# Performance work log

Measured on AMD Instinct MI355X. Metric: run time of the kernel, lower is better.

## Reference

```python
import jax, jax.numpy as jnp
import numpy as np

B, N, DIM = 8, 1024, 1024
H, DH = 16, 64           # heads, dim_head; inner_dim = H*DH = 1024
SCALE = DH ** -0.5


def setup_inputs() -> dict:
    key = jax.random.key(0)
    k_x, k_qkv, k_out, k_b = jax.random.split(key, 4)
    inner = H * DH
    x = jax.random.normal(k_x, (B, N, DIM), dtype=jnp.float32)
    # nn.Linear(dim, inner*3, bias=False): y = x @ W_qkv
    W_qkv = jax.random.normal(k_qkv, (DIM, 3 * inner), dtype=jnp.float32) * (DIM ** -0.5)
    # nn.Linear(inner, dim) with bias (project_out is True since heads!=1)
    W_out = jax.random.normal(k_out, (inner, DIM), dtype=jnp.float32) * (inner ** -0.5)
    b_out = jax.random.normal(k_b, (DIM,), dtype=jnp.float32) * 0.01
    return {"x": x, "W_qkv": W_qkv, "W_out": W_out, "b_out": b_out}


def reference(x, W_qkv, W_out, b_out):
    # 'trans' branch of Attention.forward (dropout p=0 -> identity)
    qkv = x @ W_qkv                                   # [b, n, 3*inner]
    q, k, v = jnp.split(qkv, 3, axis=-1)              # each [b, n, inner]
    def to_heads(t):
        b, n, _ = t.shape
        return t.reshape(b, n, H, DH).transpose(0, 2, 1, 3)  # [b, h, n, d]
    q, k, v = to_heads(q), to_heads(k), to_heads(v)
    dots = jnp.einsum('bhid,bhjd->bhij', q, k) * SCALE  # [b, h, n, n]
    attn = jax.nn.softmax(dots, axis=-1)
    out = jnp.einsum('bhij,bhjd->bhid', attn, v)        # [b, h, n, d]
    # original sets attn = out (b h n d) before merging heads
    attn_ret = out
    out_m = out.transpose(0, 2, 1, 3).reshape(B, N, H * DH)  # [b, n, inner]
    proj = out_m @ W_out + b_out                        # [b, n, dim]
    return (proj, attn_ret)
```

## Files before the change

### kernel.cpp

```cpp
#include <hip/hip_runtime.h>
#include <hip/hip_bf16.h>
#include <math.h>

typedef __bf16 bf16_t;
typedef __bf16 bf16x8 __attribute__((ext_vector_type(8)));
typedef __bf16 bf16x4 __attribute__((ext_vector_type(4)));
typedef float f32x4 __attribute__((ext_vector_type(4)));

#define MFMA16(a, b, c) __builtin_amdgcn_mfma_f32_16x16x32_bf16((a), (b), (c), 0, 0, 0)

#define AS3(p) ((__attribute__((address_space(3))) void*)(p))
#define AS1(p) ((const __attribute__((address_space(1))) void*)(p))

#define B_ 8
#define N_ 1024
#define DIM_ 1024
#define H_ 16
#define DH_ 64

#define QSCALE 0.18033688011112042f
#define SM_SHIFT 12.0f

__global__ __launch_bounds__(256) void k_convert(const float* __restrict__ in,
                                                 bf16_t* __restrict__ out) {
    size_t idx = ((size_t)blockIdx.x * 256 + threadIdx.x) * 8;
    f32x4 a = *(const f32x4*)(in + idx);
    f32x4 b = *(const f32x4*)(in + idx + 4);
    bf16x8 o;
    o[0] = (bf16_t)a[0]; o[1] = (bf16_t)a[1]; o[2] = (bf16_t)a[2]; o[3] = (bf16_t)a[3];
    o[4] = (bf16_t)b[0]; o[5] = (bf16_t)b[1]; o[6] = (bf16_t)b[2]; o[7] = (bf16_t)b[3];
    *(bf16x8*)(out + idx) = o;
}

__global__ __launch_bounds__(256) void k_prep_w(const float* __restrict__ Wqkv,
                                                bf16_t* __restrict__ wqkvt,
                                                const float* __restrict__ Wout,
                                                bf16_t* __restrict__ woutt) {
    __shared__ float tile[32][33];
    int bx = blockIdx.x;
    const float* in;
    bf16_t* out;
    int C, cb;
    if (bx < 96) { in = Wqkv; out = wqkvt; C = 3072; cb = bx; }
    else         { in = Wout; out = woutt; C = 1024; cb = bx - 96; }
    const int R = 1024;
    int c0 = cb * 32, r0 = blockIdx.y * 32;
    int tx = threadIdx.x, ty = threadIdx.y;
#pragma unroll
    for (int i = 0; i < 4; ++i)
        tile[ty + 8 * i][tx] = in[(size_t)(r0 + ty + 8 * i) * C + (c0 + tx)];
    __syncthreads();
#pragma unroll
    for (int i = 0; i < 4; ++i)
        out[(size_t)(c0 + ty + 8 * i) * R + (r0 + tx)] = (bf16_t)tile[tx][ty + 8 * i];
}

__global__ __launch_bounds__(512, 2) void k_gemm_qkv(const bf16_t* __restrict__ A,
                                                     const bf16_t* __restrict__ Bt,
                                                     bf16_t* __restrict__ qb,
                                                     bf16_t* __restrict__ kbuf,
                                                     bf16_t* __restrict__ vtb) {
    __shared__ __align__(16) bf16_t As[2][256 * 64];
    __shared__ __align__(16) bf16_t Bs[2][256 * 64];
    int tid = threadIdx.x;
    int lane = tid & 63, wave = tid >> 6;
    int quad = lane >> 4, l16 = lane & 15;
    int wr = wave >> 2, wc = wave & 3;

    int bid = blockIdx.x;
    int swz = (bid & 7) * 48 + (bid >> 3);
    int mt = swz / 12, nt = swz % 12;
    int m0 = mt * 256, c0 = nt * 256;

    const f32x4 vzero = {0.f, 0.f, 0.f, 0.f};
    f32x4 acc[8][4];
#pragma unroll
    for (int i = 0; i < 8; ++i)
#pragma unroll
        for (int j = 0; j < 4; ++j) acc[i][j] = vzero;

    int s0 = ((quad) ^ (l16 & 7)) * 8;
    int s1 = ((4 + quad) ^ (l16 & 7)) * 8;

    auto stage = [&](int t) {
        int k0 = t * 64;
        bf16_t* Ad = &As[t & 1][0];
        bf16_t* Bd = &Bs[t & 1][0];
#pragma unroll
        for (int i = 0; i < 4; ++i) {
            int cid = tid + 512 * i;
            int row = cid >> 3;
            int g = (cid & 7) ^ (row & 7);
            __builtin_amdgcn_global_load_lds(
                AS1(A + (size_t)(m0 + row) * 1024 + k0 + g * 8), AS3(Ad + cid * 8), 16, 0, 0);
        }
#pragma unroll
        for (int i = 0; i < 4; ++i) {
            int cid = tid + 512 * i;
            int row = cid >> 3;
            int g = (cid & 7) ^ (row & 7);
            __builtin_amdgcn_global_load_lds(
                AS1(Bt + (size_t)(c0 + row) * 1024 + k0 + g * 8), AS3(Bd + cid * 8), 16, 0, 0);
        }
    };

    stage(0);
    stage(1);

#pragma unroll 2
    for (int t = 0; t < 16; ++t) {
        int cur = t & 1;
        if (t < 15)
            asm volatile("s_waitcnt vmcnt(8)" ::: "memory");
        else
            asm volatile("s_waitcnt vmcnt(0)" ::: "memory");
        __builtin_amdgcn_s_barrier();
        asm volatile("" ::: "memory");

        const bf16_t* Arow = &As[cur][0] + (size_t)(wr * 128 + l16) * 64;
        const bf16_t* Brow = &Bs[cur][0] + (size_t)(wc * 64 + l16) * 64;

        bf16x8 af[4][2], bq0[2][2], bq1[2][2];

#pragma unroll
        for (int i = 0; i < 4; ++i) {
            af[i][0] = *(const bf16x8*)(Arow + (16 * i) * 64 + s0);
            af[i][1] = *(const bf16x8*)(Arow + (16 * i) * 64 + s1);
        }
#pragma unroll
        for (int j = 0; j < 2; ++j) {
            bq0[j][0] = *(const bf16x8*)(Brow + (16 * j) * 64 + s0);
            bq0[j][1] = *(const bf16x8*)(Brow + (16 * j) * 64 + s1);
        }
        __builtin_amdgcn_s_setprio(1);
#pragma unroll
        for (int i = 0; i < 4; ++i)
#pragma unroll
            for (int j = 0; j < 2; ++j) {
                acc[i][j] = MFMA16(af[i][0], bq0[j][0], acc[i][j]);
                acc[i][j] = MFMA16(af[i][1], bq0[j][1], acc[i][j]);
            }
        __builtin_amdgcn_s_setprio(0);

#pragma unroll
        for (int j = 0; j < 2; ++j) {
            bq1[j][0] = *(const bf16x8*)(Brow + (32 + 16 * j) * 64 + s0);
            bq1[j][1] = *(const bf16x8*)(Brow + (32 + 16 * j) * 64 + s1);
        }
        __builtin_amdgcn_s_setprio(1);
#pragma unroll
        for (int i = 0; i < 4; ++i)
#pragma unroll
            for (int j = 0; j < 2; ++j) {
                acc[i][2 + j] = MFMA16(af[i][0], bq1[j][0], acc[i][2 + j]);
                acc[i][2 + j] = MFMA16(af[i][1], bq1[j][1], acc[i][2 + j]);
            }
        __builtin_amdgcn_s_setprio(0);

#pragma unroll
        for (int i = 0; i < 4; ++i) {
            af[i][0] = *(const bf16x8*)(Arow + (64 + 16 * i) * 64 + s0);
            af[i][1] = *(const bf16x8*)(Arow + (64 + 16 * i) * 64 + s1);
        }
        __builtin_amdgcn_s_setprio(1);
#pragma unroll
        for (int i = 0; i < 4; ++i)
#pragma unroll
            for (int j = 0; j < 2; ++j) {
                acc[4 + i][2 + j] = MFMA16(af[i][0], bq1[j][0], acc[4 + i][2 + j]);
                acc[4 + i][2 + j] = MFMA16(af[i][1], bq1[j][1], acc[4 + i][2 + j]);
            }
        __builtin_amdgcn_s_setprio(0);

        __builtin_amdgcn_s_setprio(1);
#pragma unroll
        for (int i = 0; i < 4; ++i)
#pragma unroll
            for (int j = 0; j < 2; ++j) {
                acc[4 + i][j] = MFMA16(af[i][0], bq0[j][0], acc[4 + i][j]);
                acc[4 + i][j] = MFMA16(af[i][1], bq0[j][1], acc[4 + i][j]);
            }
        __builtin_amdgcn_s_setprio(0);

        asm volatile("" ::: "memory");
        __builtin_amdgcn_s_barrier();
        if (t + 2 < 16) stage(t + 2);
    }

    int tsel = nt >> 2;
#pragma unroll
    for (int i = 0; i < 8; ++i) {
#pragma unroll
        for (int r = 0; r < 4; ++r) {
            int m = m0 + wr * 128 + 16 * i + quad * 4 + r;
            int b = m >> 10, n = m & 1023;
#pragma unroll
            for (int j = 0; j < 4; ++j) {
                int cc = c0 + wc * 64 + 16 * j + l16;
                int ic = cc & 1023;
                int h = ic >> 6, d = ic & 63;
                float val = acc[i][j][r];
                if (tsel == 0)
                    qb[(((size_t)b * H_ + h) * N_ + n) * DH_ + d] = (bf16_t)(val * QSCALE);
                else if (tsel == 1)
                    kbuf[(((size_t)b * H_ + h) * N_ + n) * DH_ + d] = (bf16_t)val;
                else
                    vtb[(((size_t)b * H_ + h) * DH_ + d) * N_ + n] = (bf16_t)val;
            }
        }
    }
}

__global__ __launch_bounds__(256, 2) void k_attn(const bf16_t* __restrict__ q,
                                                 const bf16_t* __restrict__ k,
                                                 const bf16_t* __restrict__ vt,
                                                 float* __restrict__ oattn,
                                                 bf16_t* __restrict__ outm) {
    __shared__ __align__(16) bf16_t Ks[64 * 64];
    __shared__ __align__(16) bf16_t Vs[64 * 64];
    __shared__ __align__(16) bf16_t Ps[4 * 4 * 16 * 72];
    int tid = threadIdx.x;
    int lane = tid & 63, wave = tid >> 6;
    int quad = lane >> 4, l16 = lane & 15;
    int qt = blockIdx.x & 3;
    int bh = blockIdx.x >> 2;
    int b = bh >> 4, h = bh & 15;

    const bf16_t* qp = q + ((size_t)bh * N_ + qt * 256 + wave * 64) * DH_;
    bf16x8 qa[4][2];
#pragma unroll
    for (int g = 0; g < 4; ++g)
#pragma unroll
        for (int c = 0; c < 2; ++c)
            qa[g][c] = *(const bf16x8*)(qp + (size_t)(g * 16 + l16) * DH_ + c * 32 + quad * 8);

    const bf16_t* kp = k + (size_t)bh * N_ * DH_;
    const bf16_t* vp = vt + (size_t)bh * DH_ * N_;
    bf16_t* Pw = Ps + wave * (4 * 16 * 72);

    const f32x4 vzero = {0.f, 0.f, 0.f, 0.f};
    f32x4 o[4][4];
#pragma unroll
    for (int g = 0; g < 4; ++g)
#pragma unroll
        for (int t = 0; t < 4; ++t) o[g][t] = vzero;
    float lsum[4] = {0.f, 0.f, 0.f, 0.f};

    for (int kb = 0; kb < 16; ++kb) {
#pragma unroll
        for (int i = 0; i < 2; ++i) {
            int cid = tid + 256 * i;
            int row = cid >> 3;
            int g = (cid & 7) ^ (row & 7);
            __builtin_amdgcn_global_load_lds(
                AS1(kp + (size_t)(kb * 64 + row) * DH_ + g * 8), AS3(Ks + cid * 8), 16, 0, 0);
            __builtin_amdgcn_global_load_lds(
                AS1(vp + (size_t)row * N_ + kb * 64 + g * 8), AS3(Vs + cid * 8), 16, 0, 0);
        }
        __syncthreads();

        f32x4 st[4][4];
#pragma unroll
        for (int jt = 0; jt < 4; ++jt) {
#pragma unroll
            for (int g = 0; g < 4; ++g) st[g][jt] = vzero;
#pragma unroll
            for (int c = 0; c < 2; ++c) {
                int s = (4 * c + quad) ^ (l16 & 7);
                bf16x8 kf = *(const bf16x8*)(Ks + (16 * jt + l16) * 64 + s * 8);
#pragma unroll
                for (int g = 0; g < 4; ++g)
                    st[g][jt] = MFMA16(kf, qa[g][c], st[g][jt]);
            }
        }

#pragma unroll
        for (int g = 0; g < 4; ++g) {
            float ps = 0.f;
#pragma unroll
            for (int jt = 0; jt < 4; ++jt) {
                bf16x4 pk;
#pragma unroll
                for (int r = 0; r < 4; ++r) {
                    float p = __builtin_amdgcn_exp2f(st[g][jt][r] - SM_SHIFT);
                    ps += p;
                    pk[r] = (bf16_t)p;
                }
                *(bf16x4*)(Pw + g * (16 * 72) + l16 * 72 + jt * 16 + quad * 4) = pk;
            }
            lsum[g] += ps;
        }

        bf16x8 pf[4][2];
#pragma unroll
        for (int g = 0; g < 4; ++g)
#pragma unroll
            for (int c = 0; c < 2; ++c)
                pf[g][c] = *(const bf16x8*)(Pw + g * (16 * 72) + l16 * 72 + c * 32 + quad * 8);
#pragma unroll
        for (int t = 0; t < 4; ++t)
#pragma unroll
            for (int c = 0; c < 2; ++c) {
                int s = (4 * c + quad) ^ (l16 & 7);
                bf16x8 vf = *(const bf16x8*)(Vs + (16 * t + l16) * 64 + s * 8);
#pragma unroll
                for (int g = 0; g < 4; ++g)
                    o[g][t] = MFMA16(vf, pf[g][c], o[g][t]);
            }
        __syncthreads();
    }

#pragma unroll
    for (int g = 0; g < 4; ++g) {
        lsum[g] += __shfl_xor(lsum[g], 16);
        lsum[g] += __shfl_xor(lsum[g], 32);
    }

    float* Ot = (float*)Ps + wave * 16 * 68;
#pragma unroll
    for (int g = 0; g < 4; ++g) {
        float inv = 1.f / lsum[g];
#pragma unroll
        for (int t = 0; t < 4; ++t) {
            f32x4 v4;
#pragma unroll
            for (int r = 0; r < 4; ++r) v4[r] = o[g][t][r] * inv;
            *(f32x4*)(Ot + l16 * 68 + t * 16 + quad * 4) = v4;
        }
        int row = lane >> 2, cl = lane & 3;
        int n = qt * 256 + wave * 64 + g * 16 + row;
        const float* orow = Ot + row * 68 + cl * 16;
        float* gout = oattn + ((size_t)bh * N_ + n) * DH_ + cl * 16;
        bf16_t* gm = outm + ((size_t)b * N_ + n) * DIM_ + h * DH_ + cl * 16;
#pragma unroll
        for (int s = 0; s < 4; ++s) {
            f32x4 v = *(const f32x4*)(orow + s * 4);
            *(f32x4*)(gout + s * 4) = v;
            bf16x4 vb;
#pragma unroll
            for (int r = 0; r < 4; ++r) vb[r] = (bf16_t)v[r];
            *(bf16x4*)(gm + s * 4) = vb;
        }
    }
}

__global__ __launch_bounds__(256) void k_gemm_proj(const bf16_t* __restrict__ A,
                                                   const bf16_t* __restrict__ Bt,
                                                   const float* __restrict__ bias,
                                                   float* __restrict__ out) {
    __shared__ __align__(16) bf16_t As[128 * 64];
    __shared__ __align__(16) bf16_t Bs[128 * 64];
    int tid = threadIdx.x;
    int lane = tid & 63, wave = tid >> 6;
    int quad = lane >> 4, l16 = lane & 15;
    int m0 = blockIdx.y * 128, c0 = blockIdx.x * 128;
    int wm = (wave & 1) * 64, wn = (wave >> 1) * 64;

    const f32x4 vzero = {0.f, 0.f, 0.f, 0.f};
    f32x4 acc[4][4];
#pragma unroll
    for (int i = 0; i < 4; ++i)
#pragma unroll
        for (int j = 0; j < 4; ++j) acc[i][j] = vzero;

    for (int k0 = 0; k0 < 1024; k0 += 64) {
#pragma unroll
        for (int i = 0; i < 4; ++i) {
            int cid = tid + 256 * i;
            int row = cid >> 3;
            int g = (cid & 7) ^ (row & 7);
            __builtin_amdgcn_global_load_lds(
                AS1(A + (size_t)(m0 + row) * 1024 + k0 + g * 8), AS3(As + cid * 8), 16, 0, 0);
            __builtin_amdgcn_global_load_lds(
                AS1(Bt + (size_t)(c0 + row) * 1024 + k0 + g * 8), AS3(Bs + cid * 8), 16, 0, 0);
        }
        __syncthreads();
#pragma unroll
        for (int c = 0; c < 2; ++c) {
            int s = (4 * c + quad) ^ (l16 & 7);
            bf16x8 bfr[4];
#pragma unroll
            for (int j = 0; j < 4; ++j)
                bfr[j] = *(const bf16x8*)(Bs + (wn + 16 * j + l16) * 64 + s * 8);
#pragma unroll
            for (int i = 0; i < 4; ++i) {
                bf16x8 af = *(const bf16x8*)(As + (wm + 16 * i + l16) * 64 + s * 8);
#pragma unroll
                for (int j = 0; j < 4; ++j)
                    acc[i][j] = MFMA16(af, bfr[j], acc[i][j]);
            }
        }
        __syncthreads();
    }

#pragma unroll
    for (int i = 0; i < 4; ++i) {
#pragma unroll
        for (int r = 0; r < 4; ++r) {
            int m = m0 + wm + 16 * i + quad * 4 + r;
#pragma unroll
            for (int j = 0; j < 4; ++j) {
                int cc = c0 + wn + 16 * j + l16;
                out[(size_t)m * DIM_ + cc] = acc[i][j][r] + bias[cc];
            }
        }
    }
}

extern "C" void kernel_launch(void* const* d_in, const int* in_sizes, int n_in,
                              void* d_out, int out_size, void* d_ws, size_t ws_size,
                              hipStream_t stream) {
    const float* x    = (const float*)d_in[0];
    const float* Wqkv = (const float*)d_in[1];
    const float* Wout = (const float*)d_in[2];
    const float* bout = (const float*)d_in[3];

    float* proj  = (float*)d_out;
    float* oattn = proj + (size_t)B_ * N_ * DIM_;

    char* ws = (char*)d_ws;
    const size_t MB = 1024 * 1024;
    bf16_t* xb    = (bf16_t*)(ws);
    bf16_t* wqkvt = (bf16_t*)(ws + 16 * MB);
    bf16_t* woutt = (bf16_t*)(ws + 22 * MB);
    bf16_t* qb    = (bf16_t*)(ws + 24 * MB);
    bf16_t* kbuf  = (bf16_t*)(ws + 40 * MB);
    bf16_t* vtb   = (bf16_t*)(ws + 56 * MB);
    bf16_t* outm  = (bf16_t*)(ws + 72 * MB);

    k_convert<<<4096, 256, 0, stream>>>(x, xb);
    k_prep_w<<<dim3(128, 32), dim3(32, 8), 0, stream>>>(Wqkv, wqkvt, Wout, woutt);
    k_gemm_qkv<<<384, 512, 0, stream>>>(xb, wqkvt, qb, kbuf, vtb);
    k_attn<<<512, 256, 0, stream>>>(qb, kbuf, vtb, oattn, outm);
    k_gemm_proj<<<dim3(8, 64), 256, 0, stream>>>(outm, woutt, bout, proj);
}
```

Before: 278.0 us.

## Interleave QKV GEMM prefetch with MFMA phases, split V transpose, merge prep kernels

The QKV GEMM now spreads the next tile's global-to-LDS loads across its four MFMA phases, adds barriers and scheduling fences between them, and lowers the occupancy hint to one block per CU. The GEMM epilogue writes V in row-major layout like Q and K, and a separate kernel transposes V through LDS, which removes the strided scattered stores. The x conversion and weight transpose kernels are merged into one launch. In exchange the GEMM gains many extra barriers per K step, and the pipeline pays for an additional kernel plus a round trip of V through memory.

```diff
diff --git a/kernel.cpp b/kernel.cpp
--- a/kernel.cpp
+++ b/kernel.cpp
@@ -21,31 +21,35 @@
 #define QSCALE 0.18033688011112042f
 #define SM_SHIFT 12.0f
 
-__global__ __launch_bounds__(256) void k_convert(const float* __restrict__ in,
-                                                 bf16_t* __restrict__ out) {
-    size_t idx = ((size_t)blockIdx.x * 256 + threadIdx.x) * 8;
-    f32x4 a = *(const f32x4*)(in + idx);
-    f32x4 b = *(const f32x4*)(in + idx + 4);
-    bf16x8 o;
-    o[0] = (bf16_t)a[0]; o[1] = (bf16_t)a[1]; o[2] = (bf16_t)a[2]; o[3] = (bf16_t)a[3];
-    o[4] = (bf16_t)b[0]; o[5] = (bf16_t)b[1]; o[6] = (bf16_t)b[2]; o[7] = (bf16_t)b[3];
-    *(bf16x8*)(out + idx) = o;
-}
-
-__global__ __launch_bounds__(256) void k_prep_w(const float* __restrict__ Wqkv,
-                                                bf16_t* __restrict__ wqkvt,
-                                                const float* __restrict__ Wout,
-                                                bf16_t* __restrict__ woutt) {
+__global__ __launch_bounds__(256) void k_prep(const float* __restrict__ x,
+                                              bf16_t* __restrict__ xb,
+                                              const float* __restrict__ Wqkv,
+                                              bf16_t* __restrict__ wqkvt,
+                                              const float* __restrict__ Wout,
+                                              bf16_t* __restrict__ woutt) {
+    int bx = blockIdx.x;
+    int tid = threadIdx.x;
+    if (bx < 4096) {
+        size_t idx = ((size_t)bx * 256 + tid) * 8;
+        f32x4 a = *(const f32x4*)(x + idx);
+        f32x4 b = *(const f32x4*)(x + idx + 4);
+        bf16x8 o;
+        o[0] = (bf16_t)a[0]; o[1] = (bf16_t)a[1]; o[2] = (bf16_t)a[2]; o[3] = (bf16_t)a[3];
+        o[4] = (bf16_t)b[0]; o[5] = (bf16_t)b[1]; o[6] = (bf16_t)b[2]; o[7] = (bf16_t)b[3];
+        *(bf16x8*)(xb + idx) = o;
+        return;
+    }
     __shared__ float tile[32][33];
-    int bx = blockIdx.x;
+    int idx = bx - 4096;
+    int rb = idx >> 7, cbx = idx & 127;
     const float* in;
     bf16_t* out;
     int C, cb;
-    if (bx < 96) { in = Wqkv; out = wqkvt; C = 3072; cb = bx; }
-    else         { in = Wout; out = woutt; C = 1024; cb = bx - 96; }
+    if (cbx < 96) { in = Wqkv; out = wqkvt; C = 3072; cb = cbx; }
+    else          { in = Wout; out = woutt; C = 1024; cb = cbx - 96; }
     const int R = 1024;
-    int c0 = cb * 32, r0 = blockIdx.y * 32;
-    int tx = threadIdx.x, ty = threadIdx.y;
+    int c0 = cb * 32, r0 = rb * 32;
+    int tx = tid & 31, ty = tid >> 5;
 #pragma unroll
     for (int i = 0; i < 4; ++i)
         tile[ty + 8 * i][tx] = in[(size_t)(r0 + ty + 8 * i) * C + (c0 + tx)];
@@ -55,11 +59,11 @@
         out[(size_t)(c0 + ty + 8 * i) * R + (r0 + tx)] = (bf16_t)tile[tx][ty + 8 * i];
 }
 
-__global__ __launch_bounds__(512, 2) void k_gemm_qkv(const bf16_t* __restrict__ A,
+__global__ __launch_bounds__(512, 1) void k_gemm_qkv(const bf16_t* __restrict__ A,
                                                      const bf16_t* __restrict__ Bt,
                                                      bf16_t* __restrict__ qb,
                                                      bf16_t* __restrict__ kbuf,
-                                                     bf16_t* __restrict__ vtb) {
+                                                     bf16_t* __restrict__ vbuf) {
     __shared__ __align__(16) bf16_t As[2][256 * 64];
     __shared__ __align__(16) bf16_t Bs[2][256 * 64];
     int tid = threadIdx.x;
@@ -82,30 +86,33 @@
     int s0 = ((quad) ^ (l16 & 7)) * 8;
     int s1 = ((4 + quad) ^ (l16 & 7)) * 8;
 
-    auto stage = [&](int t) {
+    auto stageA = [&](int t, int i) {
         int k0 = t * 64;
         bf16_t* Ad = &As[t & 1][0];
+        int cid = tid + 512 * i;
+        int row = cid >> 3;
+        int g = (cid & 7) ^ (row & 7);
+        __builtin_amdgcn_global_load_lds(
+            AS1(A + (size_t)(m0 + row) * 1024 + k0 + g * 8), AS3(Ad + cid * 8), 16, 0, 0);
+    };
+    auto stageB = [&](int t, int i) {
+        int k0 = t * 64;
         bf16_t* Bd = &Bs[t & 1][0];
-#pragma unroll
-        for (int i = 0; i < 4; ++i) {
-            int cid = tid + 512 * i;
-            int row = cid >> 3;
-            int g = (cid & 7) ^ (row & 7);
-            __builtin_amdgcn_global_load_lds(
-                AS1(A + (size_t)(m0 + row) * 1024 + k0 + g * 8), AS3(Ad + cid * 8), 16, 0, 0);
-        }
-#pragma unroll
-        for (int i = 0; i < 4; ++i) {
-            int cid = tid + 512 * i;
-            int row = cid >> 3;
-            int g = (cid & 7) ^ (row & 7);
-            __builtin_amdgcn_global_load_lds(
-                AS1(Bt + (size_t)(c0 + row) * 1024 + k0 + g * 8), AS3(Bd + cid * 8), 16, 0, 0);
-        }
+        int cid = tid + 512 * i;
+        int row = cid >> 3;
+        int g = (cid & 7) ^ (row & 7);
+        __builtin_amdgcn_global_load_lds(
+            AS1(Bt + (size_t)(c0 + row) * 1024 + k0 + g * 8), AS3(Bd + cid * 8), 16, 0, 0);
     };
-
-    stage(0);
-    stage(1);
+    auto stage_all = [&](int t) {
+#pragma unroll
+        for (int i = 0; i < 4; ++i) stageA(t, i);
+#pragma unroll
+        for (int i = 0; i < 4; ++i) stageB(t, i);
+    };
+
+    stage_all(0);
+    stage_all(1);
 
 #pragma unroll 2
     for (int t = 0; t < 16; ++t) {
@@ -119,6 +126,7 @@
 
         const bf16_t* Arow = &As[cur][0] + (size_t)(wr * 128 + l16) * 64;
         const bf16_t* Brow = &Bs[cur][0] + (size_t)(wc * 64 + l16) * 64;
+        bool pre = (t + 2 < 16);
 
         bf16x8 af[4][2], bq0[2][2], bq1[2][2];
 
@@ -132,6 +140,10 @@
             bq0[j][0] = *(const bf16x8*)(Brow + (16 * j) * 64 + s0);
             bq0[j][1] = *(const bf16x8*)(Brow + (16 * j) * 64 + s1);
         }
+        asm volatile("" ::: "memory");
+        __builtin_amdgcn_s_barrier();
+        asm volatile("s_waitcnt lgkmcnt(0)" ::: "memory");
+        __builtin_amdgcn_sched_barrier(0);
         __builtin_amdgcn_s_setprio(1);
 #pragma unroll
         for (int i = 0; i < 4; ++i)
@@ -141,12 +153,19 @@
                 acc[i][j] = MFMA16(af[i][1], bq0[j][1], acc[i][j]);
             }
         __builtin_amdgcn_s_setprio(0);
+        asm volatile("" ::: "memory");
+        __builtin_amdgcn_s_barrier();
 
 #pragma unroll
         for (int j = 0; j < 2; ++j) {
             bq1[j][0] = *(const bf16x8*)(Brow + (32 + 16 * j) * 64 + s0);
             bq1[j][1] = *(const bf16x8*)(Brow + (32 + 16 * j) * 64 + s1);
         }
+        if (pre) { stageA(t + 2, 0); stageA(t + 2, 2); }
+        asm volatile("" ::: "memory");
+        __builtin_amdgcn_s_barrier();
+        asm volatile("s_waitcnt lgkmcnt(0)" ::: "memory");
+        __builtin_amdgcn_sched_barrier(0);
         __builtin_amdgcn_s_setprio(1);
 #pragma unroll
         for (int i = 0; i < 4; ++i)
@@ -156,12 +175,22 @@
                 acc[i][2 + j] = MFMA16(af[i][1], bq1[j][1], acc[i][2 + j]);
             }
         __builtin_amdgcn_s_setprio(0);
+        asm volatile("" ::: "memory");
+        __builtin_amdgcn_s_barrier();
 
 #pragma unroll
         for (int i = 0; i < 4; ++i) {
             af[i][0] = *(const bf16x8*)(Arow + (64 + 16 * i) * 64 + s0);
             af[i][1] = *(const bf16x8*)(Arow + (64 + 16 * i) * 64 + s1);
         }
+        if (pre) {
+#pragma unroll
+            for (int i = 0; i < 4; ++i) stageB(t + 2, i);
+        }
+        asm volatile("" ::: "memory");
+        __builtin_amdgcn_s_barrier();
+        asm volatile("s_waitcnt lgkmcnt(0)" ::: "memory");
+        __builtin_amdgcn_sched_barrier(0);
         __builtin_amdgcn_s_setprio(1);
 #pragma unroll
         for (int i = 0; i < 4; ++i)
@@ -171,7 +200,13 @@
                 acc[4 + i][2 + j] = MFMA16(af[i][1], bq1[j][1], acc[4 + i][2 + j]);
             }
         __builtin_amdgcn_s_setprio(0);
-
+        asm volatile("" ::: "memory");
+        __builtin_amdgcn_s_barrier();
+
+        if (pre) { stageA(t + 2, 1); stageA(t + 2, 3); }
+        asm volatile("" ::: "memory");
+        __builtin_amdgcn_s_barrier();
+        __builtin_amdgcn_sched_barrier(0);
         __builtin_amdgcn_s_setprio(1);
 #pragma unroll
         for (int i = 0; i < 4; ++i)
@@ -181,13 +216,13 @@
                 acc[4 + i][j] = MFMA16(af[i][1], bq0[j][1], acc[4 + i][j]);
             }
         __builtin_amdgcn_s_setprio(0);
-
-        asm volatile("" ::: "memory");
-        __builtin_amdgcn_s_barrier();
-        if (t + 2 < 16) stage(t + 2);
+        asm volatile("" ::: "memory");
+        __builtin_amdgcn_s_barrier();
     }
 
     int tsel = nt >> 2;
+    bf16_t* obase = (tsel == 0) ? qb : (tsel == 1) ? kbuf : vbuf;
+    float scl = (tsel == 0) ? QSCALE : 1.0f;
 #pragma unroll
     for (int i = 0; i < 8; ++i) {
 #pragma unroll
@@ -199,16 +234,31 @@
                 int cc = c0 + wc * 64 + 16 * j + l16;
                 int ic = cc & 1023;
                 int h = ic >> 6, d = ic & 63;
-                float val = acc[i][j][r];
-                if (tsel == 0)
-                    qb[(((size_t)b * H_ + h) * N_ + n) * DH_ + d] = (bf16_t)(val * QSCALE);
-                else if (tsel == 1)
-                    kbuf[(((size_t)b * H_ + h) * N_ + n) * DH_ + d] = (bf16_t)val;
-                else
-                    vtb[(((size_t)b * H_ + h) * DH_ + d) * N_ + n] = (bf16_t)val;
-            }
-        }
-    }
+                obase[(((size_t)b * H_ + h) * N_ + n) * DH_ + d] = (bf16_t)(acc[i][j][r] * scl);
+            }
+        }
+    }
+}
+
+__global__ __launch_bounds__(256) void k_prep_v(const bf16_t* __restrict__ in,
+                                                bf16_t* __restrict__ out) {
+    __shared__ bf16_t t[64][65];
+    int bh = blockIdx.y;
+    int n0 = blockIdx.x * 64;
+    int tid = threadIdx.x;
+    int r = tid >> 2, c = (tid & 3) * 16;
+    const bf16_t* ip = in + ((size_t)bh * N_ + n0 + r) * DH_ + c;
+    bf16x8 a = *(const bf16x8*)ip;
+    bf16x8 b2 = *(const bf16x8*)(ip + 8);
+#pragma unroll
+    for (int e = 0; e < 8; ++e) { t[r][c + e] = a[e]; t[r][c + 8 + e] = b2[e]; }
+    __syncthreads();
+    bf16x8 o1, o2;
+#pragma unroll
+    for (int e = 0; e < 8; ++e) { o1[e] = t[c + e][r]; o2[e] = t[c + 8 + e][r]; }
+    bf16_t* op = out + ((size_t)bh * DH_ + r) * N_ + n0 + c;
+    *(bf16x8*)op = o1;
+    *(bf16x8*)(op + 8) = o2;
 }
 
 __global__ __launch_bounds__(256, 2) void k_attn(const bf16_t* __restrict__ q,
@@ -427,10 +477,11 @@
     bf16_t* kbuf  = (bf16_t*)(ws + 40 * MB);
     bf16_t* vtb   = (bf16_t*)(ws + 56 * MB);
     bf16_t* outm  = (bf16_t*)(ws + 72 * MB);
-
-    k_convert<<<4096, 256, 0, stream>>>(x, xb);
-    k_prep_w<<<dim3(128, 32), dim3(32, 8), 0, stream>>>(Wqkv, wqkvt, Wout, woutt);
-    k_gemm_qkv<<<384, 512, 0, stream>>>(xb, wqkvt, qb, kbuf, vtb);
+    bf16_t* vbuf  = outm;
+
+    k_prep<<<8192, 256, 0, stream>>>(x, xb, Wqkv, wqkvt, Wout, woutt);
+    k_gemm_qkv<<<384, 512, 0, stream>>>(xb, wqkvt, qb, kbuf, vbuf);
+    k_prep_v<<<dim3(16, 128), 256, 0, stream>>>(vbuf, vtb);
     k_attn<<<512, 256, 0, stream>>>(qb, kbuf, vtb, oattn, outm);
     k_gemm_proj<<<dim3(8, 64), 256, 0, stream>>>(outm, woutt, bout, proj);
 }
```

After: 253.5 us. 8.8% less time.
